# Kernel optimization log

Measured on AMD Instinct MI355X. Metric: run time of the kernel, lower is better.

The kernel has to match this reference:

```python
import jax, jax.numpy as jnp
import numpy as np

DELTA_V = 0.5
DELTA_D = 3.0
NUM_LABELS = 5  # labels 0..4 -> C = max label = 4


def setup_inputs() -> dict:
    key = jax.random.key(0)
    k1, k2 = jax.random.split(key)
    B, E, H, W = 16, 8, 512, 1024
    pred = jax.random.normal(k1, (B, E, H, W), dtype=jnp.float32)
    instance_label = jax.random.randint(k2, (B, H, W), 0, NUM_LABELS).astype(jnp.int32)
    binary_label = (instance_label > 0).astype(jnp.float32)[:, None]  # [B,1,H,W]
    return {"pred": pred, "binary_label": binary_label, "instance_label": instance_label}


def reference(pred, binary_label, instance_label):
    # pred: [B,E,H,W], binary_label: [B,1,H,W], instance_label: [B,H,W] int
    B, E, H, W = pred.shape
    L = NUM_LABELS
    C = L - 1  # int(instance_label.max()) with labels 0..L-1
    dtype = pred.dtype

    pred_roi = binary_label * pred                                  # [B,E,H,W]
    masks = jax.nn.one_hot(instance_label, L, dtype=dtype)          # [B,H,W,L]

    counts = jnp.einsum('bhwl->bl', masks)                          # [B,L] pixels per cluster
    sums = jnp.einsum('behw,bhwl->ble', pred_roi, masks)            # [B,L,E]
    sumsq = jnp.einsum('behw,bhwl->bl', pred_roi * pred_roi, masks)  # [B,L]

    mu = sums / counts[..., None]                                   # [B,L,E] cluster means

    # torch.norm(mu - xi) is the Frobenius norm over the whole [E,Nc] cluster:
    # ||mu - xi||_F^2 = sum(mask*x^2) - Nc*||mu||^2
    frob_sq = sumsq - counts * jnp.sum(mu * mu, axis=-1)            # [B,L]
    pos = frob_sq > 0
    n = jnp.where(pos, jnp.sqrt(jnp.where(pos, frob_sq, 1.0)), 0.0)  # safe sqrt
    var = jnp.where(n > DELTA_V, (n - DELTA_V) ** 2, 0.0)           # [B,L]
    L_var = jnp.sum(var, axis=1) / C                                # [B]

    # dist term: pairs (i,j), i != j, over means of labels 0..C-1 (original loop bound)
    mu_d = mu[:, :C]                                                # [B,C,E]
    diff = mu_d[:, :, None, :] - mu_d[:, None, :, :]                # [B,C,C,E]
    dsq = jnp.sum(diff * diff, axis=-1)                             # [B,C,C]
    offdiag = (1.0 - jnp.eye(C, dtype=dtype))[None]                 # [1,C,C]
    ok = (dsq > 0) & (offdiag > 0)
    d = jnp.sqrt(jnp.where(ok, dsq, 1.0))
    hinge = jnp.where(ok, jax.nn.relu(DELTA_D - d) ** 2,
                      jnp.where(offdiag > 0, DELTA_D ** 2, 0.0))
    L_dist = jnp.sum(hinge, axis=(1, 2))                            # [B]

    return jnp.mean(L_var) + jnp.mean(L_dist)
```

## Files before the change

kernel.cpp:

```cpp
#include <hip/hip_runtime.h>

#define NB 16
#define NE 8
#define NH 512
#define NW 1024
#define HW (NH * NW)
#define CHUNKS 128
#define TPB 256
#define PIX_PER_CHUNK (HW / CHUNKS)
#define GROUPS (PIX_PER_CHUNK / (TPB * 4))
#define ACC_STRIDE 40

__global__ __launch_bounds__(TPB) void cluster_partial(
    const float* __restrict__ pred, const int* __restrict__ lab,
    float* __restrict__ acc)
{
    const int b     = blockIdx.x / CHUNKS;
    const int chunk = blockIdx.x % CHUNKS;
    const int t     = threadIdx.x;

    const float* predb = pred + (long)b * NE * HW;
    const int*   labb  = lab  + (long)b * HW;
    const int base0 = chunk * PIX_PER_CHUNK + (t << 2);

    float sums[4][NE];
    float ssq_acc[4] = {0.f, 0.f, 0.f, 0.f};
    float cnt[4]     = {0.f, 0.f, 0.f, 0.f};
#pragma unroll
    for (int l = 0; l < 4; ++l)
#pragma unroll
        for (int e = 0; e < NE; ++e) sums[l][e] = 0.f;

    int4   l4 = *reinterpret_cast<const int4*>(labb + base0);
    float4 v[NE];
#pragma unroll
    for (int e = 0; e < NE; ++e)
        v[e] = *reinterpret_cast<const float4*>(predb + (long)e * HW + base0);

#pragma unroll
    for (int g = 0; g < GROUPS; ++g) {
        int4   l4n = l4;
        float4 vn[NE];
#pragma unroll
        for (int e = 0; e < NE; ++e) vn[e] = v[e];
        if (g + 1 < GROUPS) {
            const int off = base0 + (g + 1) * (TPB * 4);
            l4n = *reinterpret_cast<const int4*>(labb + off);
#pragma unroll
            for (int e = 0; e < NE; ++e)
                vn[e] = *reinterpret_cast<const float4*>(predb + (long)e * HW + off);
        }

        const int labs[4] = {l4.x, l4.y, l4.z, l4.w};

        float m[4][4];
#pragma unroll
        for (int p = 0; p < 4; ++p)
#pragma unroll
            for (int l = 0; l < 4; ++l)
                m[p][l] = (labs[p] == l + 1) ? 1.0f : 0.0f;

        float ssq[4] = {0.f, 0.f, 0.f, 0.f};
#pragma unroll
        for (int e = 0; e < NE; ++e) {
            const float vv[4] = {v[e].x, v[e].y, v[e].z, v[e].w};
#pragma unroll
            for (int p = 0; p < 4; ++p) {
                ssq[p] = fmaf(vv[p], vv[p], ssq[p]);
#pragma unroll
                for (int l = 0; l < 4; ++l)
                    sums[l][e] = fmaf(m[p][l], vv[p], sums[l][e]);
            }
        }
#pragma unroll
        for (int p = 0; p < 4; ++p)
#pragma unroll
            for (int l = 0; l < 4; ++l) {
                ssq_acc[l] = fmaf(m[p][l], ssq[p], ssq_acc[l]);
                cnt[l] += m[p][l];
            }

        l4 = l4n;
#pragma unroll
        for (int e = 0; e < NE; ++e) v[e] = vn[e];
    }

    float vals[ACC_STRIDE];
#pragma unroll
    for (int l = 0; l < 4; ++l) {
        vals[l]     = cnt[l];
        vals[4 + l] = ssq_acc[l];
#pragma unroll
        for (int e = 0; e < NE; ++e) vals[8 + l * NE + e] = sums[l][e];
    }
#pragma unroll
    for (int i = 0; i < ACC_STRIDE; ++i) {
        float vv = vals[i];
        vv += __shfl_down(vv, 32);
        vv += __shfl_down(vv, 16);
        vv += __shfl_down(vv, 8);
        vv += __shfl_down(vv, 4);
        vv += __shfl_down(vv, 2);
        vv += __shfl_down(vv, 1);
        vals[i] = vv;
    }

    __shared__ float red[TPB / 64][ACC_STRIDE];
    const int wave = t >> 6;
    const int lane = t & 63;
    if (lane == 0) {
#pragma unroll
        for (int i = 0; i < ACC_STRIDE; ++i) red[wave][i] = vals[i];
    }
    __syncthreads();
    if (t < ACC_STRIDE) {
        float s = red[0][t] + red[1][t] + red[2][t] + red[3][t];
        atomicAdd(&acc[b * ACC_STRIDE + t], s);
    }
}

__global__ __launch_bounds__(64) void cluster_finalize(
    const float* __restrict__ acc, float* __restrict__ out)
{
    const int t = threadIdx.x;
    float Lb = 0.f;
    if (t < NB) {
        const float* a = acc + t * ACC_STRIDE;
        float mu[4][NE];
#pragma unroll
        for (int e = 0; e < NE; ++e) mu[0][e] = 0.f;

        float Lvar = 0.f;
#pragma unroll
        for (int l = 1; l <= 4; ++l) {
            const float c   = a[l - 1];
            const float ssq = a[4 + (l - 1)];
            float mloc[NE];
            float musq = 0.f;
#pragma unroll
            for (int e = 0; e < NE; ++e) {
                mloc[e] = a[8 + (l - 1) * NE + e] / c;
                musq = fmaf(mloc[e], mloc[e], musq);
            }
            const float frob = ssq - c * musq;
            const float n = (frob > 0.f) ? sqrtf(frob) : 0.f;
            const float dv = n - 0.5f;
            Lvar += (n > 0.5f) ? dv * dv : 0.f;
            if (l < 4) {
#pragma unroll
                for (int e = 0; e < NE; ++e) mu[l][e] = mloc[e];
            }
        }
        Lvar *= 0.25f;

        float Ldist = 0.f;
#pragma unroll
        for (int i = 0; i < 4; ++i)
#pragma unroll
            for (int j = i + 1; j < 4; ++j) {
                float dsq = 0.f;
#pragma unroll
                for (int e = 0; e < NE; ++e) {
                    const float d = mu[i][e] - mu[j][e];
                    dsq = fmaf(d, d, dsq);
                }
                float h;
                if (dsq > 0.f) {
                    const float d = sqrtf(dsq);
                    float r = 3.0f - d;
                    r = (r > 0.f) ? r : 0.f;
                    h = r * r;
                } else {
                    h = 9.0f;
                }
                Ldist += 2.0f * h;
            }

        Lb = (Lvar + Ldist) * (1.0f / NB);
    }
    Lb += __shfl_down(Lb, 32);
    Lb += __shfl_down(Lb, 16);
    Lb += __shfl_down(Lb, 8);
    Lb += __shfl_down(Lb, 4);
    Lb += __shfl_down(Lb, 2);
    Lb += __shfl_down(Lb, 1);
    if (t == 0) out[0] = Lb;
}

extern "C" void kernel_launch(void* const* d_in, const int* in_sizes, int n_in,
                              void* d_out, int out_size, void* d_ws, size_t ws_size,
                              hipStream_t stream) {
    const float* pred = (const float*)d_in[0];
    const int* lab = (const int*)d_in[2];
    float* out = (float*)d_out;
    float* acc = (float*)d_ws;

    hipMemsetAsync(acc, 0, NB * ACC_STRIDE * sizeof(float), stream);
    cluster_partial<<<NB * CHUNKS, TPB, 0, stream>>>(pred, lab, acc);
    cluster_finalize<<<1, 64, 0, stream>>>(acc, out);
}
```

Baseline: 394.5 us.

## Restructure partial reduction to stream embedding planes with nontemporal triple-buffered loads

The per-block loop now iterates over embedding channels instead of pixel groups. All labels are loaded up front and packed into bytes, and pred planes are fetched with nontemporal loads through a three-deep register buffer, so two channels are always in flight. The FMA-with-mask accumulation becomes select-and-add, and per-pixel squared sums are binned by label once at the end. This aims to raise memory-level parallelism and reduce cache pollution on a bandwidth-bound stream, at the cost of more live registers (buffers sized by group count), which may lower occupancy.

```diff
diff --git a/kernel.cpp b/kernel.cpp
--- a/kernel.cpp
+++ b/kernel.cpp
@@ -8,8 +8,14 @@
 #define CHUNKS 128
 #define TPB 256
 #define PIX_PER_CHUNK (HW / CHUNKS)
-#define GROUPS (PIX_PER_CHUNK / (TPB * 4))
+#define GRP (PIX_PER_CHUNK / (TPB * 4))
 #define ACC_STRIDE 40
+
+typedef float floatx4 __attribute__((ext_vector_type(4)));
+
+static __device__ __forceinline__ floatx4 nt_load4(const float* p) {
+    return __builtin_nontemporal_load(reinterpret_cast<const floatx4*>(p));
+}
 
 __global__ __launch_bounds__(TPB) void cluster_partial(
     const float* __restrict__ pred, const int* __restrict__ lab,
@@ -19,70 +25,82 @@
     const int chunk = blockIdx.x % CHUNKS;
     const int t     = threadIdx.x;
 
-    const float* predb = pred + (long)b * NE * HW;
-    const int*   labb  = lab  + (long)b * HW;
-    const int base0 = chunk * PIX_PER_CHUNK + (t << 2);
+    const float* predb = pred + (long)b * NE * HW + chunk * PIX_PER_CHUNK;
+    const int*   labb  = lab  + (long)b * HW      + chunk * PIX_PER_CHUNK;
+    const int    toff  = t << 2;
+
+    int4 L[GRP];
+#pragma unroll
+    for (int g = 0; g < GRP; ++g)
+        L[g] = *reinterpret_cast<const int4*>(labb + g * (TPB * 4) + toff);
+
+    floatx4 buf[3][GRP];
+#pragma unroll
+    for (int g = 0; g < GRP; ++g)
+        buf[0][g] = nt_load4(predb + 0l * HW + g * (TPB * 4) + toff);
+#pragma unroll
+    for (int g = 0; g < GRP; ++g)
+        buf[1][g] = nt_load4(predb + 1l * HW + g * (TPB * 4) + toff);
+
+    unsigned lp[GRP];
+    float cnt[4] = {0.f, 0.f, 0.f, 0.f};
+#pragma unroll
+    for (int g = 0; g < GRP; ++g) {
+        lp[g] = (unsigned)L[g].x | ((unsigned)L[g].y << 8) |
+                ((unsigned)L[g].z << 16) | ((unsigned)L[g].w << 24);
+        const int lbs[4] = {L[g].x, L[g].y, L[g].z, L[g].w};
+#pragma unroll
+        for (int p = 0; p < 4; ++p)
+#pragma unroll
+            for (int l = 0; l < 4; ++l)
+                cnt[l] += (lbs[p] == l + 1) ? 1.0f : 0.0f;
+    }
 
     float sums[4][NE];
+#pragma unroll
+    for (int l = 0; l < 4; ++l)
+#pragma unroll
+        for (int e = 0; e < NE; ++e) sums[l][e] = 0.f;
+    float ssqp[GRP * 4];
+#pragma unroll
+    for (int i = 0; i < GRP * 4; ++i) ssqp[i] = 0.f;
+
+#pragma unroll
+    for (int e = 0; e < NE; ++e) {
+        if (e + 2 < NE) {
+#pragma unroll
+            for (int g = 0; g < GRP; ++g)
+                buf[(e + 2) % 3][g] =
+                    nt_load4(predb + (long)(e + 2) * HW + g * (TPB * 4) + toff);
+        }
+#pragma unroll
+        for (int g = 0; g < GRP; ++g) {
+            const floatx4  v  = buf[e % 3][g];
+            const unsigned lw = lp[g];
+            const float vv[4] = {v.x, v.y, v.z, v.w};
+#pragma unroll
+            for (int p = 0; p < 4; ++p) {
+                const int   lb = (int)((lw >> (8 * p)) & 0xffu);
+                const float x  = vv[p];
+                ssqp[g * 4 + p] = fmaf(x, x, ssqp[g * 4 + p]);
+#pragma unroll
+                for (int l = 0; l < 4; ++l)
+                    sums[l][e] += (lb == l + 1) ? x : 0.0f;
+            }
+        }
+    }
+
     float ssq_acc[4] = {0.f, 0.f, 0.f, 0.f};
-    float cnt[4]     = {0.f, 0.f, 0.f, 0.f};
-#pragma unroll
-    for (int l = 0; l < 4; ++l)
-#pragma unroll
-        for (int e = 0; e < NE; ++e) sums[l][e] = 0.f;
-
-    int4   l4 = *reinterpret_cast<const int4*>(labb + base0);
-    float4 v[NE];
-#pragma unroll
-    for (int e = 0; e < NE; ++e)
-        v[e] = *reinterpret_cast<const float4*>(predb + (long)e * HW + base0);
-
-#pragma unroll
-    for (int g = 0; g < GROUPS; ++g) {
-        int4   l4n = l4;
-        float4 vn[NE];
-#pragma unroll
-        for (int e = 0; e < NE; ++e) vn[e] = v[e];
-        if (g + 1 < GROUPS) {
-            const int off = base0 + (g + 1) * (TPB * 4);
-            l4n = *reinterpret_cast<const int4*>(labb + off);
-#pragma unroll
-            for (int e = 0; e < NE; ++e)
-                vn[e] = *reinterpret_cast<const float4*>(predb + (long)e * HW + off);
-        }
-
-        const int labs[4] = {l4.x, l4.y, l4.z, l4.w};
-
-        float m[4][4];
-#pragma unroll
-        for (int p = 0; p < 4; ++p)
+#pragma unroll
+    for (int g = 0; g < GRP; ++g) {
+        const unsigned lw = lp[g];
+#pragma unroll
+        for (int p = 0; p < 4; ++p) {
+            const int lb = (int)((lw >> (8 * p)) & 0xffu);
 #pragma unroll
             for (int l = 0; l < 4; ++l)
-                m[p][l] = (labs[p] == l + 1) ? 1.0f : 0.0f;
-
-        float ssq[4] = {0.f, 0.f, 0.f, 0.f};
-#pragma unroll
-        for (int e = 0; e < NE; ++e) {
-            const float vv[4] = {v[e].x, v[e].y, v[e].z, v[e].w};
-#pragma unroll
-            for (int p = 0; p < 4; ++p) {
-                ssq[p] = fmaf(vv[p], vv[p], ssq[p]);
-#pragma unroll
-                for (int l = 0; l < 4; ++l)
-                    sums[l][e] = fmaf(m[p][l], vv[p], sums[l][e]);
-            }
-        }
-#pragma unroll
-        for (int p = 0; p < 4; ++p)
-#pragma unroll
-            for (int l = 0; l < 4; ++l) {
-                ssq_acc[l] = fmaf(m[p][l], ssq[p], ssq_acc[l]);
-                cnt[l] += m[p][l];
-            }
-
-        l4 = l4n;
-#pragma unroll
-        for (int e = 0; e < NE; ++e) v[e] = vn[e];
+                ssq_acc[l] += (lb == l + 1) ? ssqp[g * 4 + p] : 0.0f;
+        }
     }
 
     float vals[ACC_STRIDE];
@@ -195,7 +213,7 @@
     float* out = (float*)d_out;
     float* acc = (float*)d_ws;
 
-    hipMemsetAsync(acc, 0, NB * ACC_STRIDE * sizeof(float), stream);
+    (void)hipMemsetAsync(acc, 0, NB * ACC_STRIDE * sizeof(float), stream);
     cluster_partial<<<NB * CHUNKS, TPB, 0, stream>>>(pred, lab, acc);
     cluster_finalize<<<1, 64, 0, stream>>>(acc, out);
 }
```

Measured after the change: 409.5 us. 1.04x slower.

## Split partial reduction across embedding channels with one block per channel

Applied to the files above, without the earlier changes.

Each block now handles a single embedding channel of a pixel chunk, so the grid grows eightfold and every block issues all of its loads up front. Per-channel sums of x and x² go to separate atomic slots, and the finalize kernel adds up the channel sums of squares. The goal is more parallelism and memory-level concurrency on a bandwidth-bound reduction. In exchange, the label array is read eight times instead of once and there are more atomics.

```diff
diff --git a/kernel.cpp b/kernel.cpp
--- a/kernel.cpp
+++ b/kernel.cpp
@@ -5,96 +5,74 @@
 #define NH 512
 #define NW 1024
 #define HW (NH * NW)
-#define CHUNKS 128
 #define TPB 256
-#define PIX_PER_CHUNK (HW / CHUNKS)
-#define GROUPS (PIX_PER_CHUNK / (TPB * 4))
-#define ACC_STRIDE 40
+#define CH2 128
+#define PXC (HW / CH2)
+#define GRP (PXC / (TPB * 4))
+#define ACC2 68
+
+typedef float floatx4 __attribute__((ext_vector_type(4)));
 
 __global__ __launch_bounds__(TPB) void cluster_partial(
     const float* __restrict__ pred, const int* __restrict__ lab,
     float* __restrict__ acc)
 {
-    const int b     = blockIdx.x / CHUNKS;
-    const int chunk = blockIdx.x % CHUNKS;
+    const int bid   = blockIdx.x;
+    const int e     = bid & (NE - 1);
+    const int rest  = bid >> 3;
+    const int chunk = rest & (CH2 - 1);
+    const int b     = rest >> 7;
     const int t     = threadIdx.x;
 
-    const float* predb = pred + (long)b * NE * HW;
-    const int*   labb  = lab  + (long)b * HW;
-    const int base0 = chunk * PIX_PER_CHUNK + (t << 2);
+    const float* predb = pred + ((long)b * NE + e) * HW + chunk * PXC;
+    const int*   labb  = lab  + (long)b * HW           + chunk * PXC;
+    const int    toff  = t << 2;
 
-    float sums[4][NE];
-    float ssq_acc[4] = {0.f, 0.f, 0.f, 0.f};
-    float cnt[4]     = {0.f, 0.f, 0.f, 0.f};
+    int4    L[GRP];
+    floatx4 V[GRP];
 #pragma unroll
-    for (int l = 0; l < 4; ++l)
+    for (int g = 0; g < GRP; ++g)
+        L[g] = *reinterpret_cast<const int4*>(labb + g * (TPB * 4) + toff);
 #pragma unroll
-        for (int e = 0; e < NE; ++e) sums[l][e] = 0.f;
+    for (int g = 0; g < GRP; ++g)
+        V[g] = *reinterpret_cast<const floatx4*>(predb + g * (TPB * 4) + toff);
 
-    int4   l4 = *reinterpret_cast<const int4*>(labb + base0);
-    float4 v[NE];
-#pragma unroll
-    for (int e = 0; e < NE; ++e)
-        v[e] = *reinterpret_cast<const float4*>(predb + (long)e * HW + base0);
+    float cn[4] = {0.f, 0.f, 0.f, 0.f};
+    float sq[4] = {0.f, 0.f, 0.f, 0.f};
+    float se[4] = {0.f, 0.f, 0.f, 0.f};
 
 #pragma unroll
-    for (int g = 0; g < GROUPS; ++g) {
-        int4   l4n = l4;
-        float4 vn[NE];
+    for (int g = 0; g < GRP; ++g) {
+        const int lbs[4] = {L[g].x, L[g].y, L[g].z, L[g].w};
 #pragma unroll
-        for (int e = 0; e < NE; ++e) vn[e] = v[e];
-        if (g + 1 < GROUPS) {
-            const int off = base0 + (g + 1) * (TPB * 4);
-            l4n = *reinterpret_cast<const int4*>(labb + off);
+        for (int p = 0; p < 4; ++p) {
+            const float x  = V[g][p];
+            const float x2 = x * x;
 #pragma unroll
-            for (int e = 0; e < NE; ++e)
-                vn[e] = *reinterpret_cast<const float4*>(predb + (long)e * HW + off);
+            for (int l = 0; l < 4; ++l) {
+                const float m = (lbs[p] == l + 1) ? 1.0f : 0.0f;
+                se[l] = fmaf(m, x,  se[l]);
+                sq[l] = fmaf(m, x2, sq[l]);
+            }
         }
-
-        const int labs[4] = {l4.x, l4.y, l4.z, l4.w};
-
-        float m[4][4];
+        if (e == 0) {
 #pragma unroll
-        for (int p = 0; p < 4; ++p)
-#pragma unroll
-            for (int l = 0; l < 4; ++l)
-                m[p][l] = (labs[p] == l + 1) ? 1.0f : 0.0f;
-
-        float ssq[4] = {0.f, 0.f, 0.f, 0.f};
-#pragma unroll
-        for (int e = 0; e < NE; ++e) {
-            const float vv[4] = {v[e].x, v[e].y, v[e].z, v[e].w};
-#pragma unroll
-            for (int p = 0; p < 4; ++p) {
-                ssq[p] = fmaf(vv[p], vv[p], ssq[p]);
+            for (int p = 0; p < 4; ++p)
 #pragma unroll
                 for (int l = 0; l < 4; ++l)
-                    sums[l][e] = fmaf(m[p][l], vv[p], sums[l][e]);
-            }
+                    cn[l] += (lbs[p] == l + 1) ? 1.0f : 0.0f;
         }
-#pragma unroll
-        for (int p = 0; p < 4; ++p)
-#pragma unroll
-            for (int l = 0; l < 4; ++l) {
-                ssq_acc[l] = fmaf(m[p][l], ssq[p], ssq_acc[l]);
-                cnt[l] += m[p][l];
-            }
-
-        l4 = l4n;
-#pragma unroll
-        for (int e = 0; e < NE; ++e) v[e] = vn[e];
     }
 
-    float vals[ACC_STRIDE];
+    float vals[12];
 #pragma unroll
     for (int l = 0; l < 4; ++l) {
-        vals[l]     = cnt[l];
-        vals[4 + l] = ssq_acc[l];
-#pragma unroll
-        for (int e = 0; e < NE; ++e) vals[8 + l * NE + e] = sums[l][e];
+        vals[l]     = cn[l];
+        vals[4 + l] = sq[l];
+        vals[8 + l] = se[l];
     }
 #pragma unroll
-    for (int i = 0; i < ACC_STRIDE; ++i) {
+    for (int i = 0; i < 12; ++i) {
         float vv = vals[i];
         vv += __shfl_down(vv, 32);
         vv += __shfl_down(vv, 16);
@@ -105,17 +83,23 @@
         vals[i] = vv;
     }
 
-    __shared__ float red[TPB / 64][ACC_STRIDE];
+    __shared__ float red[TPB / 64][12];
     const int wave = t >> 6;
     const int lane = t & 63;
     if (lane == 0) {
 #pragma unroll
-        for (int i = 0; i < ACC_STRIDE; ++i) red[wave][i] = vals[i];
+        for (int i = 0; i < 12; ++i) red[wave][i] = vals[i];
     }
     __syncthreads();
-    if (t < ACC_STRIDE) {
-        float s = red[0][t] + red[1][t] + red[2][t] + red[3][t];
-        atomicAdd(&acc[b * ACC_STRIDE + t], s);
+    if (t < 12) {
+        const float s = red[0][t] + red[1][t] + red[2][t] + red[3][t];
+        if (t < 4) {
+            if (e == 0) atomicAdd(&acc[b * ACC2 + t], s);
+        } else if (t < 8) {
+            atomicAdd(&acc[b * ACC2 + 4  + (t - 4) * NE + e], s);
+        } else {
+            atomicAdd(&acc[b * ACC2 + 36 + (t - 8) * NE + e], s);
+        }
     }
 }
 
@@ -125,7 +109,7 @@
     const int t = threadIdx.x;
     float Lb = 0.f;
     if (t < NB) {
-        const float* a = acc + t * ACC_STRIDE;
+        const float* a = acc + t * ACC2;
         float mu[4][NE];
 #pragma unroll
         for (int e = 0; e < NE; ++e) mu[0][e] = 0.f;
@@ -133,13 +117,15 @@
         float Lvar = 0.f;
 #pragma unroll
         for (int l = 1; l <= 4; ++l) {
-            const float c   = a[l - 1];
-            const float ssq = a[4 + (l - 1)];
+            const float c = a[l - 1];
+            float ssq = 0.f;
+#pragma unroll
+            for (int e = 0; e < NE; ++e) ssq += a[4 + (l - 1) * NE + e];
             float mloc[NE];
             float musq = 0.f;
 #pragma unroll
             for (int e = 0; e < NE; ++e) {
-                mloc[e] = a[8 + (l - 1) * NE + e] / c;
+                mloc[e] = a[36 + (l - 1) * NE + e] / c;
                 musq = fmaf(mloc[e], mloc[e], musq);
             }
             const float frob = ssq - c * musq;
@@ -195,7 +181,7 @@
     float* out = (float*)d_out;
     float* acc = (float*)d_ws;
 
-    hipMemsetAsync(acc, 0, NB * ACC_STRIDE * sizeof(float), stream);
-    cluster_partial<<<NB * CHUNKS, TPB, 0, stream>>>(pred, lab, acc);
+    (void)hipMemsetAsync(acc, 0, NB * ACC2 * sizeof(float), stream);
+    cluster_partial<<<NB * CH2 * NE, TPB, 0, stream>>>(pred, lab, acc);
     cluster_finalize<<<1, 64, 0, stream>>>(acc, out);
 }
```

Result: slower. 411.0 us (+4.2%).
